# Optimization experiments

Hardware: AMD Instinct MI355X
Metric: run time of the kernel (lower is better)

The kernel has to match this reference:

```python
import jax, jax.numpy as jnp
import numpy as np

TEMP = 0.2
N_IT = 10
P = 1


def setup_inputs() -> dict:
    key = jax.random.key(0)
    N, M = 8192, 8192
    k1, _ = jax.random.split(key)
    cdist = jax.random.uniform(k1, (N, M), dtype=jnp.float32)
    A = jnp.ones((N,), dtype=jnp.float32) / N  # uniform source density
    B = jnp.ones((M,), dtype=jnp.float32) / M  # uniform target density
    return {"cdist": cdist, "A": A, "B": B}


def reference(cdist, A, B):
    N, M = cdist.shape
    # C = (cdist - cdist.min()) / cdist.std(); torch std is unbiased (ddof=1)
    C = (cdist - cdist.min()) / jnp.std(cdist, ddof=1)
    # p == 1 -> no power applied
    Q = jnp.exp(-C / TEMP)
    Q = Q / Q.sum()

    def body(i, carry):
        U, V = carry
        # T implicit as U[:,None] * Q * V; first iter T == Q since U=V=1
        T = U[:, None] * Q * V[None, :]
        V = V * (B / T.sum(axis=0))
        T = U[:, None] * Q * V[None, :]
        U = U * (A / T.sum(axis=1))
        return (U, V)

    U0 = jnp.ones((N,), dtype=cdist.dtype)
    V0 = jnp.ones((M,), dtype=cdist.dtype)
    U, V = jax.lax.fori_loop(0, N_IT, body, (U0, V0))
    T = U[:, None] * Q * V[None, :]
    return T
```

## Files before the change

kernel.cpp:

```cpp
#include <hip/hip_runtime.h>

#define TEMP_ 0.2
#define NITER 10


typedef _Float16 half_t;
struct __align__(16) H8 { half_t h[8]; };
typedef float floatx4 __attribute__((ext_vector_type(4)));

__device__ __forceinline__ float fast_rcp(float x){ return __builtin_amdgcn_rcpf(x); }

__device__ __forceinline__ float wsum(float v){
#pragma unroll
  for (int o = 32; o > 0; o >>= 1) v += __shfl_down(v, o, 64);
  return v;
}
__device__ __forceinline__ double wsumd(double v){
#pragma unroll
  for (int o = 32; o > 0; o >>= 1) v += __shfl_down(v, o, 64);
  return v;
}
__device__ __forceinline__ float wmin(float v){
#pragma unroll
  for (int o = 32; o > 0; o >>= 1) v = fminf(v, __shfl_down(v, o, 64));
  return v;
}

__device__ __forceinline__ unsigned fenc(float f){
  unsigned u = __float_as_uint(f);
  return (u & 0x80000000u) ? ~u : (u | 0x80000000u);
}
__device__ __forceinline__ float fdec(unsigned u){
  return (u & 0x80000000u) ? __uint_as_float(u & 0x7FFFFFFFu) : __uint_as_float(~u);
}

__device__ __forceinline__ void get_stats(const double* __restrict__ sums,
                                          const unsigned* __restrict__ minbits,
                                          long long NM, float& cmin, float& kscale){
  double s  = sums[0];
  double ss = sums[1];
  double mean = s / (double)NM;
  double var  = (ss - mean * s) / (double)(NM - 1);
  cmin  = fdec(*minbits);
  kscale = (float)(1.0 / (sqrt(var) * TEMP_));
}

__device__ __forceinline__ void load_vr(const float* __restrict__ cs,
                                        const float* __restrict__ B,
                                        float S, int t, float* vr){
#pragma unroll
  for (int k = 0; k < 4; ++k){
    int c = k * 2048 + t * 8;
    float4 ca = *(const float4*)(cs + c);
    float4 cb = *(const float4*)(cs + c + 4);
    float4 ba = *(const float4*)(B + c);
    float4 bb = *(const float4*)(B + c + 4);
    vr[k*8+0] = ba.x * S * fast_rcp(ca.x);
    vr[k*8+1] = ba.y * S * fast_rcp(ca.y);
    vr[k*8+2] = ba.z * S * fast_rcp(ca.z);
    vr[k*8+3] = ba.w * S * fast_rcp(ca.w);
    vr[k*8+4] = bb.x * S * fast_rcp(cb.x);
    vr[k*8+5] = bb.y * S * fast_rcp(cb.y);
    vr[k*8+6] = bb.z * S * fast_rcp(cb.z);
    vr[k*8+7] = bb.w * S * fast_rcp(cb.w);
  }
}

__global__ void k_init(double* __restrict__ sums, double* __restrict__ Ssum,
                       unsigned* __restrict__ minbits,
                       float* __restrict__ c0, float* __restrict__ c1, int M){
  int i = blockIdx.x * blockDim.x + threadIdx.x;
  if (i == 0){ sums[0] = 0.0; sums[1] = 0.0; *Ssum = 0.0; *minbits = 0xFFFFFFFFu; }
  if (i < M){ c0[i] = 0.f; c1[i] = 0.f; }
}

__global__ __launch_bounds__(256) void k_reduce(const float* __restrict__ cd, long long n4,
                                                double* __restrict__ sums,
                                                unsigned* __restrict__ minbits){
  const float4* c4 = (const float4*)cd;
  long long i0 = (long long)blockIdx.x * blockDim.x + threadIdx.x;
  long long stride = (long long)gridDim.x * blockDim.x;
  double s = 0.0, ss = 0.0;
  float  fs = 0.f, fss = 0.f;
  float  mn = __int_as_float(0x7F800000);
  int cnt = 0;
  for (long long i = i0; i < n4; i += stride){
    float4 v = c4[i];
    mn = fminf(mn, fminf(fminf(v.x, v.y), fminf(v.z, v.w)));
    fs  += (v.x + v.y) + (v.z + v.w);
    fss += v.x*v.x + v.y*v.y + v.z*v.z + v.w*v.w;
    if (++cnt == 8){ s += fs; ss += fss; fs = 0.f; fss = 0.f; cnt = 0; }
  }
  s += fs; ss += fss;
  s = wsumd(s); ss = wsumd(ss); mn = wmin(mn);
  __shared__ double lds[8];
  __shared__ float  ldm[4];
  int lane = threadIdx.x & 63, wid = threadIdx.x >> 6;
  if (lane == 0){ lds[wid] = s; lds[4 + wid] = ss; ldm[wid] = mn; }
  __syncthreads();
  if (threadIdx.x == 0){
    unsafeAtomicAdd(&sums[0], lds[0] + lds[1] + lds[2] + lds[3]);
    unsafeAtomicAdd(&sums[1], lds[4] + lds[5] + lds[6] + lds[7]);
    atomicMin(minbits, fenc(fminf(fminf(ldm[0], ldm[1]), fminf(ldm[2], ldm[3]))));
  }
}

__global__ __launch_bounds__(256) void k_expcol(const float* __restrict__ cd, half_t* __restrict__ E,
                                                const double* __restrict__ sums,
                                                const unsigned* __restrict__ minbits,
                                                float* __restrict__ colsum, double* __restrict__ Ssum,
                                                int N, int M){
  float cmin, kscale;
  get_stats(sums, minbits, (long long)N * M, cmin, kscale);
  int t = threadIdx.x;
  int c0 = blockIdx.x * 2048 + t * 8;
  int r0 = blockIdx.y * 64;
  float a0=0.f,a1=0.f,a2=0.f,a3=0.f,a4=0.f,a5=0.f,a6=0.f,a7=0.f;
#pragma unroll 4
  for (int r = 0; r < 64; ++r){
    long long idx = (long long)(r0 + r) * M + c0;
    float4 va = *(const float4*)(cd + idx);
    float4 vb = *(const float4*)(cd + idx + 4);
    float e0 = __expf((cmin - va.x) * kscale);
    float e1 = __expf((cmin - va.y) * kscale);
    float e2 = __expf((cmin - va.z) * kscale);
    float e3 = __expf((cmin - va.w) * kscale);
    float e4 = __expf((cmin - vb.x) * kscale);
    float e5 = __expf((cmin - vb.y) * kscale);
    float e6 = __expf((cmin - vb.z) * kscale);
    float e7 = __expf((cmin - vb.w) * kscale);
    H8 o;
    o.h[0]=(half_t)e0; o.h[1]=(half_t)e1; o.h[2]=(half_t)e2; o.h[3]=(half_t)e3;
    o.h[4]=(half_t)e4; o.h[5]=(half_t)e5; o.h[6]=(half_t)e6; o.h[7]=(half_t)e7;
    *(H8*)(E + idx) = o;
    a0+=e0; a1+=e1; a2+=e2; a3+=e3; a4+=e4; a5+=e5; a6+=e6; a7+=e7;
  }
  unsafeAtomicAdd(&colsum[c0+0], a0);
  unsafeAtomicAdd(&colsum[c0+1], a1);
  unsafeAtomicAdd(&colsum[c0+2], a2);
  unsafeAtomicAdd(&colsum[c0+3], a3);
  unsafeAtomicAdd(&colsum[c0+4], a4);
  unsafeAtomicAdd(&colsum[c0+5], a5);
  unsafeAtomicAdd(&colsum[c0+6], a6);
  unsafeAtomicAdd(&colsum[c0+7], a7);
  float tot = wsum(((a0+a1)+(a2+a3)) + ((a4+a5)+(a6+a7)));
  __shared__ float lt[4];
  int lane = t & 63, wid = t >> 6;
  if (lane == 0) lt[wid] = tot;
  __syncthreads();
  if (t == 0) unsafeAtomicAdd(Ssum, (double)((lt[0] + lt[1]) + (lt[2] + lt[3])));
}

__global__ __launch_bounds__(256) void k_rp(const half_t* __restrict__ E,
                                            const float* __restrict__ cs,
                                            const float* __restrict__ B,
                                            const float* __restrict__ A,
                                            const double* __restrict__ Ssum,
                                            float* __restrict__ u, int M){
  int t = threadIdx.x;
  int r0 = blockIdx.x * 8;
  float S = (float)(*Ssum);
  float vr[32];
  load_vr(cs, B, S, t, vr);
  float acc[8];
  const half_t* Eb = E + (long long)r0 * M;
#pragma unroll
  for (int r = 0; r < 8; ++r){
    float p = 0.f;
#pragma unroll
    for (int k = 0; k < 4; ++k){
      H8 hh = *(const H8*)(Eb + (long long)r * M + k * 2048 + t * 8);
      p += (float)hh.h[0]*vr[k*8+0] + (float)hh.h[1]*vr[k*8+1]
         + (float)hh.h[2]*vr[k*8+2] + (float)hh.h[3]*vr[k*8+3]
         + (float)hh.h[4]*vr[k*8+4] + (float)hh.h[5]*vr[k*8+5]
         + (float)hh.h[6]*vr[k*8+6] + (float)hh.h[7]*vr[k*8+7];
    }
    acc[r] = p;
  }
  __shared__ float lds[4][8];
  int lane = t & 63, wid = t >> 6;
#pragma unroll
  for (int r = 0; r < 8; ++r){
    float p = wsum(acc[r]);
    if (lane == 0) lds[wid][r] = p;
  }
  __syncthreads();
  if (t < 8){
    float rs = (lds[0][t] + lds[1][t]) + (lds[2][t] + lds[3][t]);
    u[r0 + t] = A[r0 + t] * S * fast_rcp(rs);
  }
}

__global__ __launch_bounds__(256) void k_cp(const half_t* __restrict__ E,
                                            const float* __restrict__ u,
                                            float* __restrict__ cs_next,
                                            float* __restrict__ cs_zero, int M){
  int t = threadIdx.x;
  int c0 = blockIdx.x * 2048 + t * 8;
  int r0 = blockIdx.y * 64;
  int bid = blockIdx.y * gridDim.x + blockIdx.x;
  int z = bid * 16 + t;
  if (t < 16 && z < M) cs_zero[z] = 0.f;
  __shared__ float ul[64];
  if (t < 64) ul[t] = u[r0 + t];
  __syncthreads();
  float a0=0.f,a1=0.f,a2=0.f,a3=0.f,a4=0.f,a5=0.f,a6=0.f,a7=0.f;
#pragma unroll 8
  for (int r = 0; r < 64; ++r){
    float ur = ul[r];
    H8 hh = *(const H8*)(E + (long long)(r0 + r) * M + c0);
    a0 += ur * (float)hh.h[0];
    a1 += ur * (float)hh.h[1];
    a2 += ur * (float)hh.h[2];
    a3 += ur * (float)hh.h[3];
    a4 += ur * (float)hh.h[4];
    a5 += ur * (float)hh.h[5];
    a6 += ur * (float)hh.h[6];
    a7 += ur * (float)hh.h[7];
  }
  unsafeAtomicAdd(&cs_next[c0+0], a0);
  unsafeAtomicAdd(&cs_next[c0+1], a1);
  unsafeAtomicAdd(&cs_next[c0+2], a2);
  unsafeAtomicAdd(&cs_next[c0+3], a3);
  unsafeAtomicAdd(&cs_next[c0+4], a4);
  unsafeAtomicAdd(&cs_next[c0+5], a5);
  unsafeAtomicAdd(&cs_next[c0+6], a6);
  unsafeAtomicAdd(&cs_next[c0+7], a7);
}

__global__ __launch_bounds__(256) void k_final_E(const half_t* __restrict__ E,
                                                 const float* __restrict__ u,
                                                 const float* __restrict__ cs,
                                                 const float* __restrict__ B,
                                                 float* __restrict__ T, int r_base, int M){
  int t = threadIdx.x;
  int r0 = r_base + blockIdx.x * 8;
  float vr[32];
  load_vr(cs, B, 1.0f, t, vr);
  for (int r = 0; r < 8; ++r){
    int row = r0 + r;
    float ur = u[row];
#pragma unroll
    for (int k = 0; k < 4; ++k){
      long long idx = (long long)row * M + k * 2048 + t * 8;
      H8 hh = *(const H8*)(E + idx);
      floatx4 oa, ob;
      oa.x = ur * vr[k*8+0] * (float)hh.h[0];
      oa.y = ur * vr[k*8+1] * (float)hh.h[1];
      oa.z = ur * vr[k*8+2] * (float)hh.h[2];
      oa.w = ur * vr[k*8+3] * (float)hh.h[3];
      ob.x = ur * vr[k*8+4] * (float)hh.h[4];
      ob.y = ur * vr[k*8+5] * (float)hh.h[5];
      ob.z = ur * vr[k*8+6] * (float)hh.h[6];
      ob.w = ur * vr[k*8+7] * (float)hh.h[7];
      __builtin_nontemporal_store(oa, (floatx4*)(T + idx));
      __builtin_nontemporal_store(ob, (floatx4*)(T + idx + 4));
    }
  }
}

__global__ __launch_bounds__(256) void k_final_cd(const float* __restrict__ cd,
                                                  const float* __restrict__ u,
                                                  const float* __restrict__ cs,
                                                  const float* __restrict__ B,
                                                  const double* __restrict__ sums,
                                                  const unsigned* __restrict__ minbits,
                                                  float* __restrict__ T, int N, int M){
  float cmin, kscale;
  get_stats(sums, minbits, (long long)N * M, cmin, kscale);
  int t = threadIdx.x;
  int r0 = blockIdx.x * 8;
  float vr[32];
  load_vr(cs, B, 1.0f, t, vr);
  for (int r = 0; r < 8; ++r){
    int row = r0 + r;
    float ur = u[row];
#pragma unroll
    for (int k = 0; k < 4; ++k){
      long long idx = (long long)row * M + k * 2048 + t * 8;
      float4 a = *(const float4*)(cd + idx);
      float4 b = *(const float4*)(cd + idx + 4);
      floatx4 oa, ob;
      oa.x = ur * vr[k*8+0] * __expf((cmin - a.x) * kscale);
      oa.y = ur * vr[k*8+1] * __expf((cmin - a.y) * kscale);
      oa.z = ur * vr[k*8+2] * __expf((cmin - a.z) * kscale);
      oa.w = ur * vr[k*8+3] * __expf((cmin - a.w) * kscale);
      ob.x = ur * vr[k*8+4] * __expf((cmin - b.x) * kscale);
      ob.y = ur * vr[k*8+5] * __expf((cmin - b.y) * kscale);
      ob.z = ur * vr[k*8+6] * __expf((cmin - b.z) * kscale);
      ob.w = ur * vr[k*8+7] * __expf((cmin - b.w) * kscale);
      __builtin_nontemporal_store(oa, (floatx4*)(T + idx));
      __builtin_nontemporal_store(ob, (floatx4*)(T + idx + 4));
    }
  }
}

extern "C" void kernel_launch(void* const* d_in, const int* in_sizes, int n_in,
                              void* d_out, int out_size, void* d_ws, size_t ws_size,
                              hipStream_t stream){
  const float* cd = (const float*)d_in[0];
  const float* A  = (const float*)d_in[1];
  const float* B  = (const float*)d_in[2];
  int N = in_sizes[1];
  int M = in_sizes[2];
  float*  T = (float*)d_out;
  half_t* E = (half_t*)d_out;

  char* ws = (char*)d_ws;
  double*   sums    = (double*)ws;
  double*   Ssum    = (double*)(ws + 16);
  unsigned* minbits = (unsigned*)(ws + 24);
  float*    c0      = (float*)(ws + 32);
  float*    c1      = c0 + M;
  float*    u       = c1 + M;

  long long n4 = (long long)N * M / 4;

  k_init<<<(M + 255) / 256, 256, 0, stream>>>(sums, Ssum, minbits, c0, c1, M);
  k_reduce<<<2048, 256, 0, stream>>>(cd, n4, sums, minbits);
  k_expcol<<<dim3(M / 2048, N / 64), 256, 0, stream>>>(cd, E, sums, minbits, c0, Ssum, N, M);

  for (int it = 0; it < NITER; ++it){
    float* cur = (it & 1) ? c1 : c0;
    float* nxt = (it & 1) ? c0 : c1;
    k_rp<<<N / 8, 256, 0, stream>>>(E, cur, B, A, Ssum, u, M);
    if (it + 1 < NITER)
      k_cp<<<dim3(M / 2048, N / 64), 256, 0, stream>>>(E, u, nxt, cur, M);
  }
  float* csl = ((NITER - 1) & 1) ? c1 : c0;

  k_final_E<<<(N / 2) / 8, 256, 0, stream>>>(E, u, csl, B, T, N / 2, M);
  k_final_E<<<(N / 4) / 8, 256, 0, stream>>>(E, u, csl, B, T, N / 4, M);
  k_final_cd<<<(N / 4) / 8, 256, 0, stream>>>(cd, u, csl, B, sums, minbits, T, N, M);
}
```

Measured before the change: 1.353 ms.

## Fuse whole Sinkhorn pipeline into one persistent cooperative kernel with fused row/col pass

Replaces the chain of many kernel launches with a single cooperative persistent kernel that uses grid.sync between phases: stats reduction, exp/colsum, iterations, and final output. Each iteration now fuses the row-sum and column-sum passes, so E is read once per iteration instead of twice, with per-thread column accumulators flushed by atomics and a triple-buffered colsum. The grid is capped at 512 blocks, which risks lower memory-level parallelism, and adds per-row __syncthreads and grid-wide barriers. The multi-launch path is kept as a fallback if the cooperative launch fails.

```diff
diff --git a/kernel.cpp b/kernel.cpp
--- a/kernel.cpp
+++ b/kernel.cpp
@@ -1,4 +1,7 @@
 #include <hip/hip_runtime.h>
+#include <hip/hip_cooperative_groups.h>
+
+namespace cg = cooperative_groups;
 
 #define TEMP_ 0.2
 #define NITER 10
@@ -27,11 +30,11 @@
 }
 
 __device__ __forceinline__ unsigned fenc(float f){
-  unsigned u = __float_as_uint(f);
-  return (u & 0x80000000u) ? ~u : (u | 0x80000000u);
-}
-__device__ __forceinline__ float fdec(unsigned u){
-  return (u & 0x80000000u) ? __uint_as_float(u & 0x7FFFFFFFu) : __uint_as_float(~u);
+  unsigned x = __float_as_uint(f);
+  return (x & 0x80000000u) ? ~x : (x | 0x80000000u);
+}
+__device__ __forceinline__ float fdec(unsigned x){
+  return (x & 0x80000000u) ? __uint_as_float(x & 0x7FFFFFFFu) : __uint_as_float(~x);
 }
 
 __device__ __forceinline__ void get_stats(const double* __restrict__ sums,
@@ -66,59 +69,70 @@
   }
 }
 
-__global__ void k_init(double* __restrict__ sums, double* __restrict__ Ssum,
-                       unsigned* __restrict__ minbits,
-                       float* __restrict__ c0, float* __restrict__ c1, int M){
-  int i = blockIdx.x * blockDim.x + threadIdx.x;
-  if (i == 0){ sums[0] = 0.0; sums[1] = 0.0; *Ssum = 0.0; *minbits = 0xFFFFFFFFu; }
-  if (i < M){ c0[i] = 0.f; c1[i] = 0.f; }
-}
-
-__global__ __launch_bounds__(256) void k_reduce(const float* __restrict__ cd, long long n4,
-                                                double* __restrict__ sums,
-                                                unsigned* __restrict__ minbits){
-  const float4* c4 = (const float4*)cd;
-  long long i0 = (long long)blockIdx.x * blockDim.x + threadIdx.x;
-  long long stride = (long long)gridDim.x * blockDim.x;
-  double s = 0.0, ss = 0.0;
-  float  fs = 0.f, fss = 0.f;
-  float  mn = __int_as_float(0x7F800000);
-  int cnt = 0;
-  for (long long i = i0; i < n4; i += stride){
-    float4 v = c4[i];
-    mn = fminf(mn, fminf(fminf(v.x, v.y), fminf(v.z, v.w)));
-    fs  += (v.x + v.y) + (v.z + v.w);
-    fss += v.x*v.x + v.y*v.y + v.z*v.z + v.w*v.w;
-    if (++cnt == 8){ s += fs; ss += fss; fs = 0.f; fss = 0.f; cnt = 0; }
-  }
-  s += fs; ss += fss;
-  s = wsumd(s); ss = wsumd(ss); mn = wmin(mn);
-  __shared__ double lds[8];
-  __shared__ float  ldm[4];
-  int lane = threadIdx.x & 63, wid = threadIdx.x >> 6;
-  if (lane == 0){ lds[wid] = s; lds[4 + wid] = ss; ldm[wid] = mn; }
-  __syncthreads();
-  if (threadIdx.x == 0){
-    unsafeAtomicAdd(&sums[0], lds[0] + lds[1] + lds[2] + lds[3]);
-    unsafeAtomicAdd(&sums[1], lds[4] + lds[5] + lds[6] + lds[7]);
-    atomicMin(minbits, fenc(fminf(fminf(ldm[0], ldm[1]), fminf(ldm[2], ldm[3]))));
-  }
-}
-
-__global__ __launch_bounds__(256) void k_expcol(const float* __restrict__ cd, half_t* __restrict__ E,
-                                                const double* __restrict__ sums,
-                                                const unsigned* __restrict__ minbits,
-                                                float* __restrict__ colsum, double* __restrict__ Ssum,
-                                                int N, int M){
-  float cmin, kscale;
-  get_stats(sums, minbits, (long long)N * M, cmin, kscale);
-  int t = threadIdx.x;
-  int c0 = blockIdx.x * 2048 + t * 8;
-  int r0 = blockIdx.y * 64;
+__device__ __forceinline__ void final_rows_E(const half_t* __restrict__ E,
+                                             const float* __restrict__ u,
+                                             const float* vr, float* __restrict__ T,
+                                             int r0, int M, int t){
+  for (int r = 0; r < 8; ++r){
+    int row = r0 + r;
+    float ur = u[row];
+#pragma unroll
+    for (int k = 0; k < 4; ++k){
+      long long idx = (long long)row * M + k * 2048 + t * 8;
+      H8 hh = *(const H8*)(E + idx);
+      floatx4 oa, ob;
+      oa.x = ur * vr[k*8+0] * (float)hh.h[0];
+      oa.y = ur * vr[k*8+1] * (float)hh.h[1];
+      oa.z = ur * vr[k*8+2] * (float)hh.h[2];
+      oa.w = ur * vr[k*8+3] * (float)hh.h[3];
+      ob.x = ur * vr[k*8+4] * (float)hh.h[4];
+      ob.y = ur * vr[k*8+5] * (float)hh.h[5];
+      ob.z = ur * vr[k*8+6] * (float)hh.h[6];
+      ob.w = ur * vr[k*8+7] * (float)hh.h[7];
+      __builtin_nontemporal_store(oa, (floatx4*)(T + idx));
+      __builtin_nontemporal_store(ob, (floatx4*)(T + idx + 4));
+    }
+  }
+}
+
+__device__ __forceinline__ void final_rows_cd(const float* __restrict__ cd,
+                                              const float* __restrict__ u,
+                                              const float* vr, float* __restrict__ T,
+                                              int r0, int M, int t,
+                                              float cmin, float kscale){
+  for (int r = 0; r < 8; ++r){
+    int row = r0 + r;
+    float ur = u[row];
+#pragma unroll
+    for (int k = 0; k < 4; ++k){
+      long long idx = (long long)row * M + k * 2048 + t * 8;
+      float4 a = *(const float4*)(cd + idx);
+      float4 b = *(const float4*)(cd + idx + 4);
+      floatx4 oa, ob;
+      oa.x = ur * vr[k*8+0] * __expf((cmin - a.x) * kscale);
+      oa.y = ur * vr[k*8+1] * __expf((cmin - a.y) * kscale);
+      oa.z = ur * vr[k*8+2] * __expf((cmin - a.z) * kscale);
+      oa.w = ur * vr[k*8+3] * __expf((cmin - a.w) * kscale);
+      ob.x = ur * vr[k*8+4] * __expf((cmin - b.x) * kscale);
+      ob.y = ur * vr[k*8+5] * __expf((cmin - b.y) * kscale);
+      ob.z = ur * vr[k*8+6] * __expf((cmin - b.z) * kscale);
+      ob.w = ur * vr[k*8+7] * __expf((cmin - b.w) * kscale);
+      __builtin_nontemporal_store(oa, (floatx4*)(T + idx));
+      __builtin_nontemporal_store(ob, (floatx4*)(T + idx + 4));
+    }
+  }
+}
+
+__device__ __forceinline__ float expcol_tile(const float* __restrict__ cd,
+                                             half_t* __restrict__ E,
+                                             float* __restrict__ colsum,
+                                             int bx, int by, int M, int t,
+                                             float cmin, float kscale){
+  int cc = bx * 2048 + t * 8;
+  int r0 = by * 64;
   float a0=0.f,a1=0.f,a2=0.f,a3=0.f,a4=0.f,a5=0.f,a6=0.f,a7=0.f;
-#pragma unroll 4
   for (int r = 0; r < 64; ++r){
-    long long idx = (long long)(r0 + r) * M + c0;
+    long long idx = (long long)(r0 + r) * M + cc;
     float4 va = *(const float4*)(cd + idx);
     float4 vb = *(const float4*)(cd + idx + 4);
     float e0 = __expf((cmin - va.x) * kscale);
@@ -135,53 +149,233 @@
     *(H8*)(E + idx) = o;
     a0+=e0; a1+=e1; a2+=e2; a3+=e3; a4+=e4; a5+=e5; a6+=e6; a7+=e7;
   }
-  unsafeAtomicAdd(&colsum[c0+0], a0);
-  unsafeAtomicAdd(&colsum[c0+1], a1);
-  unsafeAtomicAdd(&colsum[c0+2], a2);
-  unsafeAtomicAdd(&colsum[c0+3], a3);
-  unsafeAtomicAdd(&colsum[c0+4], a4);
-  unsafeAtomicAdd(&colsum[c0+5], a5);
-  unsafeAtomicAdd(&colsum[c0+6], a6);
-  unsafeAtomicAdd(&colsum[c0+7], a7);
-  float tot = wsum(((a0+a1)+(a2+a3)) + ((a4+a5)+(a6+a7)));
+  unsafeAtomicAdd(&colsum[cc+0], a0);
+  unsafeAtomicAdd(&colsum[cc+1], a1);
+  unsafeAtomicAdd(&colsum[cc+2], a2);
+  unsafeAtomicAdd(&colsum[cc+3], a3);
+  unsafeAtomicAdd(&colsum[cc+4], a4);
+  unsafeAtomicAdd(&colsum[cc+5], a5);
+  unsafeAtomicAdd(&colsum[cc+6], a6);
+  unsafeAtomicAdd(&colsum[cc+7], a7);
+  return ((a0+a1)+(a2+a3)) + ((a4+a5)+(a6+a7));
+}
+
+__global__ __launch_bounds__(256, 2) void k_iter(
+    const float* __restrict__ cd, const float* __restrict__ A, const float* __restrict__ B,
+    half_t* __restrict__ E, float* __restrict__ T,
+    double* __restrict__ sums, unsigned* __restrict__ minbits, double* __restrict__ Ssum,
+    float* __restrict__ c0a, float* __restrict__ c1a, float* __restrict__ c2a,
+    float* __restrict__ u, int N, int M)
+{
+  cg::grid_group grid = cg::this_grid();
+  const int t   = threadIdx.x;
+  const int bid = blockIdx.x;
+  const int nb  = gridDim.x;
+  const long long NM = (long long)N * M;
+
+  __shared__ double sdl[8];
+  __shared__ float  sfl[8];
+  __shared__ float  lred[2][4];
+
+  {
+    const float4* c4 = (const float4*)cd;
+    long long n4 = NM >> 2;
+    long long stride = (long long)nb * 256;
+    double s = 0.0, ss = 0.0;
+    float fs = 0.f, fss = 0.f;
+    float mn = __int_as_float(0x7F800000);
+    int cnt = 0;
+    for (long long i = (long long)bid * 256 + t; i < n4; i += stride){
+      float4 v = c4[i];
+      mn = fminf(mn, fminf(fminf(v.x, v.y), fminf(v.z, v.w)));
+      fs  += (v.x + v.y) + (v.z + v.w);
+      fss += v.x*v.x + v.y*v.y + v.z*v.z + v.w*v.w;
+      if (++cnt == 8){ s += fs; ss += fss; fs = 0.f; fss = 0.f; cnt = 0; }
+    }
+    s += fs; ss += fss;
+    s = wsumd(s); ss = wsumd(ss); mn = wmin(mn);
+    int lane = t & 63, wid = t >> 6;
+    if (lane == 0){ sdl[wid] = s; sdl[4 + wid] = ss; sfl[wid] = mn; }
+    __syncthreads();
+    if (t == 0){
+      unsafeAtomicAdd(&sums[0], (sdl[0] + sdl[1]) + (sdl[2] + sdl[3]));
+      unsafeAtomicAdd(&sums[1], (sdl[4] + sdl[5]) + (sdl[6] + sdl[7]));
+      atomicMin(minbits, fenc(fminf(fminf(sfl[0], sfl[1]), fminf(sfl[2], sfl[3]))));
+    }
+  }
+  grid.sync();
+
+  float cmin, kscale;
+  get_stats(sums, minbits, NM, cmin, kscale);
+
+  {
+    int tw = M / 2048;
+    int ntiles = tw * (N / 64);
+    for (int tile = bid; tile < ntiles; tile += nb){
+      float tot = expcol_tile(cd, E, c0a, tile % tw, tile / tw, M, t, cmin, kscale);
+      tot = wsum(tot);
+      int lane = t & 63, wid = t >> 6;
+      if (lane == 0) sfl[4 + wid] = tot;
+      __syncthreads();
+      if (t == 0) unsafeAtomicAdd(Ssum, (double)((sfl[4] + sfl[5]) + (sfl[6] + sfl[7])));
+      __syncthreads();
+    }
+  }
+  grid.sync();
+
+  const float S = (float)(*Ssum);
+  float* csb[3] = {c0a, c1a, c2a};
+
+  for (int it = 0; it < NITER; ++it){
+    const float* R = csb[it % 3];
+    float*       W = csb[(it + 1) % 3];
+    float*       Z = csb[(it + 2) % 3];
+    const bool last = (it == NITER - 1);
+
+    float vr[32];
+    load_vr(R, B, S, t, vr);
+    float acc[32];
+#pragma unroll
+    for (int c = 0; c < 32; ++c) acc[c] = 0.f;
+
+    int nch = N / 16;
+    for (int ch = bid; ch < nch; ch += nb){
+      int r0 = ch * 16;
+      for (int r = 0; r < 16; ++r){
+        int row = r0 + r;
+        const half_t* Er = E + (long long)row * M;
+        float hf[32];
+        float p = 0.f;
+#pragma unroll
+        for (int k = 0; k < 4; ++k){
+          H8 hh = *(const H8*)(Er + k * 2048 + t * 8);
+#pragma unroll
+          for (int j = 0; j < 8; ++j){
+            float f = (float)hh.h[j];
+            hf[k*8+j] = f;
+            p += f * vr[k*8+j];
+          }
+        }
+#pragma unroll
+        for (int o = 32; o > 0; o >>= 1) p += __shfl_xor(p, o, 64);
+        if ((t & 63) == 0) lred[r & 1][t >> 6] = p;
+        __syncthreads();
+        float rs = (lred[r & 1][0] + lred[r & 1][1]) + (lred[r & 1][2] + lred[r & 1][3]);
+        float ui = A[row] * S * fast_rcp(rs);
+        if (last){
+          if (t == 0) u[row] = ui;
+        } else {
+#pragma unroll
+          for (int c = 0; c < 32; ++c) acc[c] += hf[c] * ui;
+        }
+      }
+    }
+    if (!last){
+#pragma unroll
+      for (int k = 0; k < 4; ++k)
+#pragma unroll
+        for (int j = 0; j < 8; ++j)
+          unsafeAtomicAdd(&W[k * 2048 + t * 8 + j], acc[k*8+j]);
+      for (int z = bid * 256 + t; z < M; z += nb * 256) Z[z] = 0.f;
+    }
+    grid.sync();
+  }
+
+  {
+    float vr[32];
+    load_vr(csb[(NITER - 1) % 3], B, 1.0f, t, vr);
+    for (int ch = bid; ch < (N / 2) / 8; ch += nb)
+      final_rows_E(E, u, vr, T, N / 2 + ch * 8, M, t);
+    grid.sync();
+    for (int ch = bid; ch < (N / 4) / 8; ch += nb)
+      final_rows_E(E, u, vr, T, N / 4 + ch * 8, M, t);
+    grid.sync();
+    for (int ch = bid; ch < (N / 4) / 8; ch += nb)
+      final_rows_cd(cd, u, vr, T, ch * 8, M, t, cmin, kscale);
+  }
+}
+
+__global__ void k_init(double* __restrict__ sums, double* __restrict__ Ssum,
+                       unsigned* __restrict__ minbits,
+                       float* __restrict__ c0, float* __restrict__ c1,
+                       float* __restrict__ c2, int M){
+  int i = blockIdx.x * blockDim.x + threadIdx.x;
+  if (i == 0){ sums[0] = 0.0; sums[1] = 0.0; *Ssum = 0.0; *minbits = 0xFFFFFFFFu; }
+  if (i < M){ c0[i] = 0.f; c1[i] = 0.f; c2[i] = 0.f; }
+}
+
+__global__ __launch_bounds__(256) void k_reduce(const float* __restrict__ cd, long long n4,
+                                                double* __restrict__ sums,
+                                                unsigned* __restrict__ minbits){
+  const float4* c4 = (const float4*)cd;
+  long long i0 = (long long)blockIdx.x * blockDim.x + threadIdx.x;
+  long long stride = (long long)gridDim.x * blockDim.x;
+  double s = 0.0, ss = 0.0;
+  float fs = 0.f, fss = 0.f;
+  float mn = __int_as_float(0x7F800000);
+  int cnt = 0;
+  for (long long i = i0; i < n4; i += stride){
+    float4 v = c4[i];
+    mn = fminf(mn, fminf(fminf(v.x, v.y), fminf(v.z, v.w)));
+    fs  += (v.x + v.y) + (v.z + v.w);
+    fss += v.x*v.x + v.y*v.y + v.z*v.z + v.w*v.w;
+    if (++cnt == 8){ s += fs; ss += fss; fs = 0.f; fss = 0.f; cnt = 0; }
+  }
+  s += fs; ss += fss;
+  s = wsumd(s); ss = wsumd(ss); mn = wmin(mn);
+  __shared__ double lds[8];
+  __shared__ float  ldm[4];
+  int lane = threadIdx.x & 63, wid = threadIdx.x >> 6;
+  if (lane == 0){ lds[wid] = s; lds[4 + wid] = ss; ldm[wid] = mn; }
+  __syncthreads();
+  if (threadIdx.x == 0){
+    unsafeAtomicAdd(&sums[0], lds[0] + lds[1] + lds[2] + lds[3]);
+    unsafeAtomicAdd(&sums[1], lds[4] + lds[5] + lds[6] + lds[7]);
+    atomicMin(minbits, fenc(fminf(fminf(ldm[0], ldm[1]), fminf(ldm[2], ldm[3]))));
+  }
+}
+
+__global__ __launch_bounds__(256) void k_expcol(const float* __restrict__ cd, half_t* __restrict__ E,
+                                                const double* __restrict__ sums,
+                                                const unsigned* __restrict__ minbits,
+                                                float* __restrict__ colsum, double* __restrict__ Ssum,
+                                                int N, int M){
+  float cmin, kscale;
+  get_stats(sums, minbits, (long long)N * M, cmin, kscale);
+  float tot = expcol_tile(cd, E, colsum, blockIdx.x, blockIdx.y, M, threadIdx.x, cmin, kscale);
+  tot = wsum(tot);
   __shared__ float lt[4];
-  int lane = t & 63, wid = t >> 6;
+  int lane = threadIdx.x & 63, wid = threadIdx.x >> 6;
   if (lane == 0) lt[wid] = tot;
   __syncthreads();
-  if (t == 0) unsafeAtomicAdd(Ssum, (double)((lt[0] + lt[1]) + (lt[2] + lt[3])));
-}
-
-__global__ __launch_bounds__(256) void k_rp(const half_t* __restrict__ E,
-                                            const float* __restrict__ cs,
-                                            const float* __restrict__ B,
-                                            const float* __restrict__ A,
-                                            const double* __restrict__ Ssum,
-                                            float* __restrict__ u, int M){
+  if (threadIdx.x == 0) unsafeAtomicAdd(Ssum, (double)((lt[0] + lt[1]) + (lt[2] + lt[3])));
+}
+
+__global__ __launch_bounds__(256) void k_rp_fb(const half_t* __restrict__ E,
+                                               const float* __restrict__ cs,
+                                               const float* __restrict__ B,
+                                               const float* __restrict__ A,
+                                               const double* __restrict__ Ssum,
+                                               float* __restrict__ u, int M){
   int t = threadIdx.x;
   int r0 = blockIdx.x * 8;
   float S = (float)(*Ssum);
   float vr[32];
   load_vr(cs, B, S, t, vr);
-  float acc[8];
-  const half_t* Eb = E + (long long)r0 * M;
-#pragma unroll
+  __shared__ float lds[4][8];
+  int lane = t & 63, wid = t >> 6;
   for (int r = 0; r < 8; ++r){
+    const half_t* Er = E + (long long)(r0 + r) * M;
     float p = 0.f;
 #pragma unroll
     for (int k = 0; k < 4; ++k){
-      H8 hh = *(const H8*)(Eb + (long long)r * M + k * 2048 + t * 8);
+      H8 hh = *(const H8*)(Er + k * 2048 + t * 8);
       p += (float)hh.h[0]*vr[k*8+0] + (float)hh.h[1]*vr[k*8+1]
          + (float)hh.h[2]*vr[k*8+2] + (float)hh.h[3]*vr[k*8+3]
          + (float)hh.h[4]*vr[k*8+4] + (float)hh.h[5]*vr[k*8+5]
          + (float)hh.h[6]*vr[k*8+6] + (float)hh.h[7]*vr[k*8+7];
     }
-    acc[r] = p;
-  }
-  __shared__ float lds[4][8];
-  int lane = t & 63, wid = t >> 6;
-#pragma unroll
-  for (int r = 0; r < 8; ++r){
-    float p = wsum(acc[r]);
+    p = wsum(p);
     if (lane == 0) lds[wid][r] = p;
   }
   __syncthreads();
@@ -191,23 +385,20 @@
   }
 }
 
-__global__ __launch_bounds__(256) void k_cp(const half_t* __restrict__ E,
-                                            const float* __restrict__ u,
-                                            float* __restrict__ cs_next,
-                                            float* __restrict__ cs_zero, int M){
+__global__ __launch_bounds__(256) void k_cp_fb(const half_t* __restrict__ E,
+                                               const float* __restrict__ u,
+                                               float* __restrict__ cs_next,
+                                               float* __restrict__ cs_zero, int M){
   int t = threadIdx.x;
   int c0 = blockIdx.x * 2048 + t * 8;
   int r0 = blockIdx.y * 64;
   int bid = blockIdx.y * gridDim.x + blockIdx.x;
   int z = bid * 16 + t;
   if (t < 16 && z < M) cs_zero[z] = 0.f;
-  __shared__ float ul[64];
-  if (t < 64) ul[t] = u[r0 + t];
-  __syncthreads();
   float a0=0.f,a1=0.f,a2=0.f,a3=0.f,a4=0.f,a5=0.f,a6=0.f,a7=0.f;
-#pragma unroll 8
+#pragma unroll 4
   for (int r = 0; r < 64; ++r){
-    float ur = ul[r];
+    float ur = u[r0 + r];
     H8 hh = *(const H8*)(E + (long long)(r0 + r) * M + c0);
     a0 += ur * (float)hh.h[0];
     a1 += ur * (float)hh.h[1];
@@ -228,71 +419,30 @@
   unsafeAtomicAdd(&cs_next[c0+7], a7);
 }
 
-__global__ __launch_bounds__(256) void k_final_E(const half_t* __restrict__ E,
-                                                 const float* __restrict__ u,
-                                                 const float* __restrict__ cs,
-                                                 const float* __restrict__ B,
-                                                 float* __restrict__ T, int r_base, int M){
+__global__ __launch_bounds__(256) void k_final_E_fb(const half_t* __restrict__ E,
+                                                    const float* __restrict__ u,
+                                                    const float* __restrict__ cs,
+                                                    const float* __restrict__ B,
+                                                    float* __restrict__ T, int r_base, int M){
   int t = threadIdx.x;
-  int r0 = r_base + blockIdx.x * 8;
   float vr[32];
   load_vr(cs, B, 1.0f, t, vr);
-  for (int r = 0; r < 8; ++r){
-    int row = r0 + r;
-    float ur = u[row];
-#pragma unroll
-    for (int k = 0; k < 4; ++k){
-      long long idx = (long long)row * M + k * 2048 + t * 8;
-      H8 hh = *(const H8*)(E + idx);
-      floatx4 oa, ob;
-      oa.x = ur * vr[k*8+0] * (float)hh.h[0];
-      oa.y = ur * vr[k*8+1] * (float)hh.h[1];
-      oa.z = ur * vr[k*8+2] * (float)hh.h[2];
-      oa.w = ur * vr[k*8+3] * (float)hh.h[3];
-      ob.x = ur * vr[k*8+4] * (float)hh.h[4];
-      ob.y = ur * vr[k*8+5] * (float)hh.h[5];
-      ob.z = ur * vr[k*8+6] * (float)hh.h[6];
-      ob.w = ur * vr[k*8+7] * (float)hh.h[7];
-      __builtin_nontemporal_store(oa, (floatx4*)(T + idx));
-      __builtin_nontemporal_store(ob, (floatx4*)(T + idx + 4));
-    }
-  }
-}
-
-__global__ __launch_bounds__(256) void k_final_cd(const float* __restrict__ cd,
-                                                  const float* __restrict__ u,
-                                                  const float* __restrict__ cs,
-                                                  const float* __restrict__ B,
-                                                  const double* __restrict__ sums,
-                                                  const unsigned* __restrict__ minbits,
-                                                  float* __restrict__ T, int N, int M){
+  final_rows_E(E, u, vr, T, r_base + blockIdx.x * 8, M, t);
+}
+
+__global__ __launch_bounds__(256) void k_final_cd_fb(const float* __restrict__ cd,
+                                                     const float* __restrict__ u,
+                                                     const float* __restrict__ cs,
+                                                     const float* __restrict__ B,
+                                                     const double* __restrict__ sums,
+                                                     const unsigned* __restrict__ minbits,
+                                                     float* __restrict__ T, int N, int M){
   float cmin, kscale;
   get_stats(sums, minbits, (long long)N * M, cmin, kscale);
   int t = threadIdx.x;
-  int r0 = blockIdx.x * 8;
   float vr[32];
   load_vr(cs, B, 1.0f, t, vr);
-  for (int r = 0; r < 8; ++r){
-    int row = r0 + r;
-    float ur = u[row];
-#pragma unroll
-    for (int k = 0; k < 4; ++k){
-      long long idx = (long long)row * M + k * 2048 + t * 8;
-      float4 a = *(const float4*)(cd + idx);
-      float4 b = *(const float4*)(cd + idx + 4);
-      floatx4 oa, ob;
-      oa.x = ur * vr[k*8+0] * __expf((cmin - a.x) * kscale);
-      oa.y = ur * vr[k*8+1] * __expf((cmin - a.y) * kscale);
-      oa.z = ur * vr[k*8+2] * __expf((cmin - a.z) * kscale);
-      oa.w = ur * vr[k*8+3] * __expf((cmin - a.w) * kscale);
-      ob.x = ur * vr[k*8+4] * __expf((cmin - b.x) * kscale);
-      ob.y = ur * vr[k*8+5] * __expf((cmin - b.y) * kscale);
-      ob.z = ur * vr[k*8+6] * __expf((cmin - b.z) * kscale);
-      ob.w = ur * vr[k*8+7] * __expf((cmin - b.w) * kscale);
-      __builtin_nontemporal_store(oa, (floatx4*)(T + idx));
-      __builtin_nontemporal_store(ob, (floatx4*)(T + idx + 4));
-    }
-  }
+  final_rows_cd(cd, u, vr, T, blockIdx.x * 8, M, t, cmin, kscale);
 }
 
 extern "C" void kernel_launch(void* const* d_in, const int* in_sizes, int n_in,
@@ -312,24 +462,41 @@
   unsigned* minbits = (unsigned*)(ws + 24);
   float*    c0      = (float*)(ws + 32);
   float*    c1      = c0 + M;
-  float*    u       = c1 + M;
+  float*    c2      = c1 + M;
+  float*    uu      = c2 + M;
 
   long long n4 = (long long)N * M / 4;
 
-  k_init<<<(M + 255) / 256, 256, 0, stream>>>(sums, Ssum, minbits, c0, c1, M);
+  k_init<<<(M + 255) / 256, 256, 0, stream>>>(sums, Ssum, minbits, c0, c1, c2, M);
+
+  int maxb = 0;
+  hipError_t oe = hipOccupancyMaxActiveBlocksPerMultiprocessor(&maxb, k_iter, 256, 0);
+  int nb = (oe == hipSuccess && maxb > 0) ? maxb * 256 : 256;
+  if (nb > 512) nb = 512;
+
+  const float* cdp = cd; const float* Ap = A; const float* Bp = B;
+  half_t* Ep = E; float* Tp = T;
+  double* sumsp = sums; unsigned* mbp = minbits; double* Ssp = Ssum;
+  float *c0p = c0, *c1p = c1, *c2p = c2, *up = uu;
+  int Nv = N, Mv = M;
+  void* args[] = {&cdp, &Ap, &Bp, &Ep, &Tp, &sumsp, &mbp, &Ssp,
+                  &c0p, &c1p, &c2p, &up, &Nv, &Mv};
+  hipError_t ce = hipLaunchCooperativeKernel((const void*)k_iter, dim3(nb), dim3(256),
+                                             args, 0, stream);
+  if (ce == hipSuccess) return;
+  (void)hipGetLastError();
+
   k_reduce<<<2048, 256, 0, stream>>>(cd, n4, sums, minbits);
   k_expcol<<<dim3(M / 2048, N / 64), 256, 0, stream>>>(cd, E, sums, minbits, c0, Ssum, N, M);
-
   for (int it = 0; it < NITER; ++it){
     float* cur = (it & 1) ? c1 : c0;
     float* nxt = (it & 1) ? c0 : c1;
-    k_rp<<<N / 8, 256, 0, stream>>>(E, cur, B, A, Ssum, u, M);
+    k_rp_fb<<<N / 8, 256, 0, stream>>>(E, cur, B, A, Ssum, uu, M);
     if (it + 1 < NITER)
-      k_cp<<<dim3(M / 2048, N / 64), 256, 0, stream>>>(E, u, nxt, cur, M);
+      k_cp_fb<<<dim3(M / 2048, N / 64), 256, 0, stream>>>(E, uu, nxt, cur, M);
   }
   float* csl = ((NITER - 1) & 1) ? c1 : c0;
-
-  k_final_E<<<(N / 2) / 8, 256, 0, stream>>>(E, u, csl, B, T, N / 2, M);
-  k_final_E<<<(N / 4) / 8, 256, 0, stream>>>(E, u, csl, B, T, N / 4, M);
-  k_final_cd<<<(N / 4) / 8, 256, 0, stream>>>(cd, u, csl, B, sums, minbits, T, N, M);
-}
+  k_final_E_fb<<<(N / 2) / 8, 256, 0, stream>>>(E, uu, csl, B, T, N / 2, M);
+  k_final_E_fb<<<(N / 4) / 8, 256, 0, stream>>>(E, uu, csl, B, T, N / 4, M);
+  k_final_cd_fb<<<(N / 4) / 8, 256, 0, stream>>>(cd, uu, csl, B, sums, minbits, T, N, M);
+}
```

New measurement: 2.357 ms. +74.2%, slower.
